# Kernel optimization log

Hardware: AMD Instinct MI355X
Metric: run time of the kernel (lower is better)

## Reference

```python
import jax, jax.numpy as jnp
import numpy as np

N = 65536
E = 1048576
NFEAT, NHID, NCLASS = 128, 64, 40


def setup_inputs() -> dict:
    key = jax.random.key(0)
    ks = jax.random.split(key, 20)
    inp = {
        "x": jax.random.normal(ks[0], (N, NFEAT), dtype=jnp.float32),
        "src": jax.random.randint(ks[1], (E,), 0, N, dtype=jnp.int32),
        "dst": jax.random.randint(ks[2], (E,), 0, N, dtype=jnp.int32),
        "edge_w": jax.random.uniform(ks[3], (E,), dtype=jnp.float32),
    }
    dims = [(NFEAT, NHID)] + [(NHID, NHID)] * 5 + [(NHID, NCLASS)]
    for i, (fi, fo) in enumerate(dims, start=1):
        scale = 1.0 / np.sqrt(fi)
        inp[f"W{i}"] = jax.random.uniform(ks[3 + i], (fi, fo), minval=-scale, maxval=scale, dtype=jnp.float32)
        inp[f"b{i}"] = jax.random.uniform(ks[10 + i], (fo,), minval=-scale, maxval=scale, dtype=jnp.float32)
    return inp


def _gc(h, W, b, src, dst, edge_w):
    # GraphConvolution: adj @ (h @ W) + b, with adj in COO form.
    support = h @ W                      # [N, fo] dense GEMM
    msgs = support[src] * edge_w[:, None]  # [E, fo] irregular gather
    agg = jax.ops.segment_sum(msgs, dst, num_segments=N)  # scatter-add
    return agg + b


def reference(x, src, dst, edge_w, W1, b1, W2, b2, W3, b3, W4, b4, W5, b5, W6, b6, W7, b7):
    # eval mode: dropout is identity
    h = jax.nn.relu(_gc(x, W1, b1, src, dst, edge_w))
    h = jax.nn.relu(_gc(h, W2, b2, src, dst, edge_w))
    h = jax.nn.relu(_gc(h, W3, b3, src, dst, edge_w)) + h
    h = jax.nn.relu(_gc(h, W4, b4, src, dst, edge_w)) + h
    h = jax.nn.relu(_gc(h, W5, b5, src, dst, edge_w)) + h
    h = jax.nn.relu(_gc(h, W6, b6, src, dst, edge_w))
    h = _gc(h, W7, b7, src, dst, edge_w)
    return jax.nn.log_softmax(h, axis=1)
```

## Files before the change

### kernel.cpp

```cpp
#include <hip/hip_runtime.h>
#include <math.h>


constexpr int NFEAT = 128, NHID = 64, NCLASS = 40;

typedef unsigned short ushort_t;
typedef int ivec4 __attribute__((ext_vector_type(4)));

__device__ inline float bf2f(ushort_t u) {
  union { unsigned int i; float f; } v; v.i = ((unsigned int)u) << 16; return v.f;
}
__device__ inline ushort_t f2bf(float f) {
  union { float f; unsigned int i; } v; v.f = f;
  unsigned int lsb = (v.i >> 16) & 1u;
  v.i += 0x7fffu + lsb;
  return (ushort_t)(v.i >> 16);
}

__global__ void rank_k(const int* __restrict__ dst, int* __restrict__ cnt4,
                       int* __restrict__ rank, int E, int N) {
  int i = blockIdx.x * blockDim.x + threadIdx.x;
  int base = i * 4;
  if (base >= E) return;
  int4 d4 = *(const int4*)(dst + base);
  int r0 = atomicAdd(&cnt4[0 * N + d4.x], 1);
  int r1 = atomicAdd(&cnt4[1 * N + d4.y], 1);
  int r2 = atomicAdd(&cnt4[2 * N + d4.z], 1);
  int r3 = atomicAdd(&cnt4[3 * N + d4.w], 1);
  ivec4 rr = { (r0 << 2) | 0, (r1 << 2) | 1, (r2 << 2) | 2, (r3 << 2) | 3 };
  __builtin_nontemporal_store(rr, (ivec4*)(rank + base));
}

__global__ void scan1_k(const int* __restrict__ cnt4, int* __restrict__ off,
                        int* __restrict__ bsum, int4* __restrict__ sb4, int n) {
  __shared__ int tmp[256];
  int tid = threadIdx.x;
  int i = blockIdx.x * 256 + tid;
  int c0 = 0, c1 = 0, c2 = 0, c3 = 0;
  if (i < n) {
    c0 = cnt4[i]; c1 = cnt4[n + i]; c2 = cnt4[2 * n + i]; c3 = cnt4[3 * n + i];
  }
  int v = c0 + c1 + c2 + c3;
  tmp[tid] = v;
  __syncthreads();
  for (int d = 1; d < 256; d <<= 1) {
    int t = (tid >= d) ? tmp[tid - d] : 0;
    __syncthreads();
    tmp[tid] += t;
    __syncthreads();
  }
  if (i < n) {
    off[i] = tmp[tid] - v;
    sb4[i] = make_int4(0, c0, c0 + c1, c0 + c1 + c2);
  }
  if (tid == 255) bsum[blockIdx.x] = tmp[255];
}

__global__ void scan2_k(int* __restrict__ bsum, int nb) {
  __shared__ int tmp[256];
  int tid = threadIdx.x;
  int v = (tid < nb) ? bsum[tid] : 0;
  tmp[tid] = v;
  __syncthreads();
  for (int d = 1; d < 256; d <<= 1) {
    int t = (tid >= d) ? tmp[tid - d] : 0;
    __syncthreads();
    tmp[tid] += t;
    __syncthreads();
  }
  if (tid < nb) bsum[tid] = tmp[tid] - v;
}

__global__ void scan3_k(int* __restrict__ off, const int* __restrict__ bsum, int n, int E) {
  int i = blockIdx.x * blockDim.x + threadIdx.x;
  if (i < n) off[i] += bsum[i >> 8];
  if (i == 0) off[n] = E;
}

__global__ void fill_k(const int* __restrict__ src, const int* __restrict__ dst,
                       const float* __restrict__ w, const int* __restrict__ off,
                       const int* __restrict__ rank, const int* __restrict__ sb4,
                       int2* __restrict__ edata, int E) {
  int i = blockIdx.x * blockDim.x + threadIdx.x;
  int base = i * 4;
  if (base >= E) return;
  int4 s4 = *(const int4*)(src + base);
  int4 d4 = *(const int4*)(dst + base);
  float4 w4 = *(const float4*)(w + base);
  int4 r4 = *(const int4*)(rank + base);
  int dd[4] = { d4.x, d4.y, d4.z, d4.w };
  int rr[4] = { r4.x, r4.y, r4.z, r4.w };
  int ss[4] = { s4.x, s4.y, s4.z, s4.w };
  float ww[4] = { w4.x, w4.y, w4.z, w4.w };
  int ob[4], sb[4];
#pragma unroll
  for (int k = 0; k < 4; ++k) ob[k] = off[dd[k]];
#pragma unroll
  for (int k = 0; k < 4; ++k) sb[k] = sb4[dd[k] * 4 + (rr[k] & 3)];
#pragma unroll
  for (int k = 0; k < 4; ++k) {
    int pos = ob[k] + sb[k] + (rr[k] >> 2);
    int2 v = make_int2(ss[k], __float_as_int(ww[k]));
    __builtin_nontemporal_store(*(const long long*)&v, (long long*)&edata[pos]);
  }
}

template<int FI, int FO>
__global__ __launch_bounds__(256) void gemm_k(const float* __restrict__ h,
                                              const float* __restrict__ W,
                                              ushort_t* __restrict__ out, int n) {
  constexpr int HS = 68;
  __shared__ float hl[64 * HS];
  __shared__ float wl[64 * 64];
  int tid = threadIdx.x;
  int row0 = blockIdx.x * 64;
  int tx = tid & 15, ty = tid >> 4;

  float acc[4][4] = {};

  for (int kc = 0; kc < FI; kc += 64) {
    {
      const float* hb = h + (size_t)row0 * FI + kc;
      for (int i = tid; i < 64 * 16; i += 256) {
        int r = i >> 4, kk = (i & 15) << 2;
        float4 v = *(const float4*)(hb + (size_t)r * FI + kk);
        *(float4*)&hl[r * HS + kk] = v;
      }
    }
    if (FO == 64) {
      const float4* Wb = (const float4*)(W + (size_t)kc * 64);
      for (int i = tid; i < 64 * 16; i += 256) ((float4*)wl)[i] = Wb[i];
    } else {
      for (int i = tid; i < 64 * 64; i += 256) wl[i] = 0.0f;
      __syncthreads();
      for (int i = tid; i < 64 * FO; i += 256)
        wl[(i / FO) * 64 + (i % FO)] = W[(size_t)(kc + i / FO) * FO + (i % FO)];
    }
    __syncthreads();

    for (int k4 = 0; k4 < 64; k4 += 4) {
      float4 a[4];
#pragma unroll
      for (int r = 0; r < 4; ++r)
        a[r] = *(const float4*)&hl[(ty * 4 + r) * HS + k4];
#pragma unroll
      for (int j = 0; j < 4; ++j) {
        float4 bv = *(const float4*)&wl[(k4 + j) * 64 + tx * 4];
        const float* bp = (const float*)&bv;
#pragma unroll
        for (int r = 0; r < 4; ++r) {
          const float* ap = (const float*)&a[r];
#pragma unroll
          for (int c = 0; c < 4; ++c) acc[r][c] += ap[j] * bp[c];
        }
      }
    }
    __syncthreads();
  }

  if (FO == 64) {
#pragma unroll
    for (int r = 0; r < 4; ++r) {
      ushort_t pk[4];
#pragma unroll
      for (int c = 0; c < 4; ++c) pk[c] = f2bf(acc[r][c]);
      *(ushort4*)&out[(size_t)(row0 + ty * 4 + r) * 64 + tx * 4] =
          make_ushort4(pk[0], pk[1], pk[2], pk[3]);
    }
  } else {
#pragma unroll
    for (int r = 0; r < 4; ++r)
#pragma unroll
      for (int c = 0; c < 4; ++c) {
        int col = tx * 4 + c;
        if (col < FO) out[(size_t)(row0 + ty * 4 + r) * FO + col] = f2bf(acc[r][c]);
      }
  }
}

__global__ __launch_bounds__(256, 4) void agg_k(
    const ushort_t* __restrict__ support,
    const int2* __restrict__ edata,
    const int* __restrict__ off,
    const float* __restrict__ bias,
    const float* __restrict__ resid,
    float* __restrict__ out,
    int n, int do_relu) {
  int tid = blockIdx.x * blockDim.x + threadIdx.x;
  int p = tid >> 6, lane = tid & 63;
  int nA = 2 * p, nB = 2 * p + 1;
  if (nA >= n) return;
  int half = lane >> 5;
  int hl   = lane & 31;
  int e0a = __builtin_amdgcn_readfirstlane(off[nA]);
  int e0b = __builtin_amdgcn_readfirstlane(off[nB]);
  int e1b = __builtin_amdgcn_readfirstlane(off[nB + 1]);
  int degA = e0b - e0a, degB = e1b - e0b;

  const ushort_t* sp = support + hl * 2;
  const int* epA = (const int*)(edata + e0a);
  const int* epB = (const int*)(edata + e0b);

  float axA[4] = {}, ayA[4] = {}, axB[4] = {}, ayB[4] = {};

  int sA[16], sB[16];
#pragma unroll
  for (int j = 0; j < 16; ++j) {
    int rel = 2 * j + half;
    sA[j] = epA[(rel < degA ? rel : 0) * 2];
  }
#pragma unroll
  for (int j = 0; j < 16; ++j) {
    int rel = 2 * j + half;
    sB[j] = epB[(rel < degB ? rel : 0) * 2];
  }
  unsigned int uA[16], uB[16];
#pragma unroll
  for (int j = 0; j < 16; ++j)
    uA[j] = *(const unsigned int*)(sp + ((size_t)sA[j] << 6));
#pragma unroll
  for (int j = 0; j < 16; ++j)
    uB[j] = *(const unsigned int*)(sp + ((size_t)sB[j] << 6));
#pragma unroll
  for (int j = 0; j < 16; ++j) {
    int rel = 2 * j + half;
    float w = (rel < degA) ? __int_as_float(epA[rel * 2 + 1]) : 0.0f;
    axA[j & 3] += w * __int_as_float(uA[j] << 16);
    ayA[j & 3] += w * __int_as_float(uA[j] & 0xffff0000u);
  }
#pragma unroll
  for (int j = 0; j < 16; ++j) {
    int rel = 2 * j + half;
    float w = (rel < degB) ? __int_as_float(epB[rel * 2 + 1]) : 0.0f;
    axB[j & 3] += w * __int_as_float(uB[j] << 16);
    ayB[j & 3] += w * __int_as_float(uB[j] & 0xffff0000u);
  }
  for (int it = 32; it < degA; it += 16) {
    int2 ed[8];
#pragma unroll
    for (int j = 0; j < 8; ++j) {
      int rel = it + 2 * j + half;
      ed[j] = *(const int2*)(epA + (rel < degA ? rel : 0) * 2);
    }
    unsigned int uu[8];
#pragma unroll
    for (int j = 0; j < 8; ++j)
      uu[j] = *(const unsigned int*)(sp + ((size_t)ed[j].x << 6));
#pragma unroll
    for (int j = 0; j < 8; ++j) {
      int rel = it + 2 * j + half;
      float w = (rel < degA) ? __int_as_float(ed[j].y) : 0.0f;
      axA[j & 3] += w * __int_as_float(uu[j] << 16);
      ayA[j & 3] += w * __int_as_float(uu[j] & 0xffff0000u);
    }
  }
  for (int it = 32; it < degB; it += 16) {
    int2 ed[8];
#pragma unroll
    for (int j = 0; j < 8; ++j) {
      int rel = it + 2 * j + half;
      ed[j] = *(const int2*)(epB + (rel < degB ? rel : 0) * 2);
    }
    unsigned int uu[8];
#pragma unroll
    for (int j = 0; j < 8; ++j)
      uu[j] = *(const unsigned int*)(sp + ((size_t)ed[j].x << 6));
#pragma unroll
    for (int j = 0; j < 8; ++j) {
      int rel = it + 2 * j + half;
      float w = (rel < degB) ? __int_as_float(ed[j].y) : 0.0f;
      axB[j & 3] += w * __int_as_float(uu[j] << 16);
      ayB[j & 3] += w * __int_as_float(uu[j] & 0xffff0000u);
    }
  }

  float sxA = ((axA[0] + axA[1]) + (axA[2] + axA[3]));
  float syA = ((ayA[0] + ayA[1]) + (ayA[2] + ayA[3]));
  float sxB = ((axB[0] + axB[1]) + (axB[2] + axB[3]));
  float syB = ((ayB[0] + ayB[1]) + (ayB[2] + ayB[3]));
  sxA += __shfl_xor(sxA, 32, 64);
  syA += __shfl_xor(syA, 32, 64);
  sxB += __shfl_xor(sxB, 32, 64);
  syB += __shfl_xor(syB, 32, 64);

  float2 bv = *(const float2*)&bias[hl * 2];
  if (half == 0) {
    float vx = sxA + bv.x, vy = syA + bv.y;
    if (do_relu) { vx = fmaxf(vx, 0.0f); vy = fmaxf(vy, 0.0f); }
    if (resid) {
      float2 r = *(const float2*)&resid[(size_t)nA * 64 + hl * 2];
      vx += r.x; vy += r.y;
    }
    *(float2*)&out[(size_t)nA * 64 + hl * 2] = make_float2(vx, vy);
  } else {
    float vx = sxB + bv.x, vy = syB + bv.y;
    if (do_relu) { vx = fmaxf(vx, 0.0f); vy = fmaxf(vy, 0.0f); }
    if (resid) {
      float2 r = *(const float2*)&resid[(size_t)nB * 64 + hl * 2];
      vx += r.x; vy += r.y;
    }
    *(float2*)&out[(size_t)nB * 64 + hl * 2] = make_float2(vx, vy);
  }
}

__global__ __launch_bounds__(256, 4) void agg_final_k(
    const ushort_t* __restrict__ support,
    const int2* __restrict__ edata,
    const int* __restrict__ off,
    const float* __restrict__ bias,
    float* __restrict__ out, int n) {
  int tid = blockIdx.x * blockDim.x + threadIdx.x;
  int p = tid >> 6, lane = tid & 63;
  int nA = 2 * p, nB = 2 * p + 1;
  if (nA >= n) return;
  int half = lane >> 5;
  int hl   = lane & 31;
  int col  = (hl < 20 ? hl : 0) * 2;
  int e0a = __builtin_amdgcn_readfirstlane(off[nA]);
  int e0b = __builtin_amdgcn_readfirstlane(off[nB]);
  int e1b = __builtin_amdgcn_readfirstlane(off[nB + 1]);
  int degA = e0b - e0a, degB = e1b - e0b;

  const ushort_t* sp = support + col;
  const int* epA = (const int*)(edata + e0a);
  const int* epB = (const int*)(edata + e0b);

  float axA[4] = {}, ayA[4] = {}, axB[4] = {}, ayB[4] = {};

  int sA[16], sB[16];
#pragma unroll
  for (int j = 0; j < 16; ++j) {
    int rel = 2 * j + half;
    sA[j] = epA[(rel < degA ? rel : 0) * 2];
  }
#pragma unroll
  for (int j = 0; j < 16; ++j) {
    int rel = 2 * j + half;
    sB[j] = epB[(rel < degB ? rel : 0) * 2];
  }
  unsigned int uA[16], uB[16];
#pragma unroll
  for (int j = 0; j < 16; ++j)
    uA[j] = *(const unsigned int*)(sp + (size_t)sA[j] * NCLASS);
#pragma unroll
  for (int j = 0; j < 16; ++j)
    uB[j] = *(const unsigned int*)(sp + (size_t)sB[j] * NCLASS);
#pragma unroll
  for (int j = 0; j < 16; ++j) {
    int rel = 2 * j + half;
    float w = (rel < degA) ? __int_as_float(epA[rel * 2 + 1]) : 0.0f;
    axA[j & 3] += w * __int_as_float(uA[j] << 16);
    ayA[j & 3] += w * __int_as_float(uA[j] & 0xffff0000u);
  }
#pragma unroll
  for (int j = 0; j < 16; ++j) {
    int rel = 2 * j + half;
    float w = (rel < degB) ? __int_as_float(epB[rel * 2 + 1]) : 0.0f;
    axB[j & 3] += w * __int_as_float(uB[j] << 16);
    ayB[j & 3] += w * __int_as_float(uB[j] & 0xffff0000u);
  }
  for (int it = 32; it < degA; it += 16) {
    int2 ed[8];
#pragma unroll
    for (int j = 0; j < 8; ++j) {
      int rel = it + 2 * j + half;
      ed[j] = *(const int2*)(epA + (rel < degA ? rel : 0) * 2);
    }
    unsigned int uu[8];
#pragma unroll
    for (int j = 0; j < 8; ++j)
      uu[j] = *(const unsigned int*)(sp + (size_t)ed[j].x * NCLASS);
#pragma unroll
    for (int j = 0; j < 8; ++j) {
      int rel = it + 2 * j + half;
      float w = (rel < degA) ? __int_as_float(ed[j].y) : 0.0f;
      axA[j & 3] += w * __int_as_float(uu[j] << 16);
      ayA[j & 3] += w * __int_as_float(uu[j] & 0xffff0000u);
    }
  }
  for (int it = 32; it < degB; it += 16) {
    int2 ed[8];
#pragma unroll
    for (int j = 0; j < 8; ++j) {
      int rel = it + 2 * j + half;
      ed[j] = *(const int2*)(epB + (rel < degB ? rel : 0) * 2);
    }
    unsigned int uu[8];
#pragma unroll
    for (int j = 0; j < 8; ++j)
      uu[j] = *(const unsigned int*)(sp + (size_t)ed[j].x * NCLASS);
#pragma unroll
    for (int j = 0; j < 8; ++j) {
      int rel = it + 2 * j + half;
      float w = (rel < degB) ? __int_as_float(ed[j].y) : 0.0f;
      axB[j & 3] += w * __int_as_float(uu[j] << 16);
      ayB[j & 3] += w * __int_as_float(uu[j] & 0xffff0000u);
    }
  }

  float sxA = ((axA[0] + axA[1]) + (axA[2] + axA[3]));
  float syA = ((ayA[0] + ayA[1]) + (ayA[2] + ayA[3]));
  float sxB = ((axB[0] + axB[1]) + (axB[2] + axB[3]));
  float syB = ((ayB[0] + ayB[1]) + (ayB[2] + ayB[3]));
  sxA += __shfl_xor(sxA, 32, 64);
  syA += __shfl_xor(syA, 32, 64);
  sxB += __shfl_xor(sxB, 32, 64);
  syB += __shfl_xor(syB, 32, 64);

  bool valid = (hl < 20);
  float2 bv = *(const float2*)&bias[col];
  float vxA = sxA + bv.x, vyA = syA + bv.y;
  float vxB = sxB + bv.x, vyB = syB + bv.y;

  float mA = valid ? fmaxf(vxA, vyA) : -INFINITY;
  float mB = valid ? fmaxf(vxB, vyB) : -INFINITY;
#pragma unroll
  for (int d = 32; d; d >>= 1) {
    mA = fmaxf(mA, __shfl_xor(mA, d, 64));
    mB = fmaxf(mB, __shfl_xor(mB, d, 64));
  }
  float exA = (valid && half == 0) ? (expf(vxA - mA) + expf(vyA - mA)) : 0.0f;
  float exB = (valid && half == 0) ? (expf(vxB - mB) + expf(vyB - mB)) : 0.0f;
  float sA2 = exA, sB2 = exB;
#pragma unroll
  for (int d = 32; d; d >>= 1) {
    sA2 += __shfl_xor(sA2, d, 64);
    sB2 += __shfl_xor(sB2, d, 64);
  }
  if (valid) {
    if (half == 0) {
      float ls = logf(sA2);
      *(float2*)&out[(size_t)nA * NCLASS + hl * 2] =
          make_float2(vxA - mA - ls, vyA - mA - ls);
    } else {
      float ls = logf(sB2);
      *(float2*)&out[(size_t)nB * NCLASS + hl * 2] =
          make_float2(vxB - mB - ls, vyB - mB - ls);
    }
  }
}

extern "C" void kernel_launch(void* const* d_in, const int* in_sizes, int n_in,
                              void* d_out, int out_size, void* d_ws, size_t ws_size,
                              hipStream_t stream) {
  const float* x   = (const float*)d_in[0];
  const int*   src = (const int*)d_in[1];
  const int*   dst = (const int*)d_in[2];
  const float* ew  = (const float*)d_in[3];
  const float* W[7]; const float* b[7];
  for (int i = 0; i < 7; ++i) {
    W[i] = (const float*)d_in[4 + 2 * i];
    b[i] = (const float*)d_in[5 + 2 * i];
  }
  int N = in_sizes[0] / NFEAT;
  int E = in_sizes[1];

  char* ws = (char*)d_ws;
  int*      off     = (int*)(ws + 0);
  int*      bsum    = (int*)(ws + (1ll << 20));
  int*      cnt4    = (int*)(ws + (2ll << 20));
  int4*     sb4     = (int4*)(ws + (3ll << 20));
  int2*     edata   = (int2*)(ws + (4ll << 20));
  int*      rank    = (int*)(ws + (12ll << 20));
  ushort_t* support = (ushort_t*)(ws + (16ll << 20));
  float*    hA      = (float*)(ws + (32ll << 20));
  float*    hB      = (float*)(ws + (48ll << 20));

  (void)hipMemsetAsync(cnt4, 0, (size_t)4 * N * sizeof(int), stream);
  rank_k<<<(E / 4 + 255) / 256, 256, 0, stream>>>(dst, cnt4, rank, E, N);
  int nb = (N + 255) / 256;
  scan1_k<<<nb, 256, 0, stream>>>(cnt4, off, bsum, sb4, N);
  scan2_k<<<1, 256, 0, stream>>>(bsum, nb);
  scan3_k<<<nb, 256, 0, stream>>>(off, bsum, N, E);
  fill_k<<<(E / 4 + 255) / 256, 256, 0, stream>>>(src, dst, ew, off, rank,
                                                  (const int*)sb4, edata, E);

  int gb_gemm = N / 64;
  int gb_agg  = N / 8;

  gemm_k<128, 64><<<gb_gemm, 256, 0, stream>>>(x, W[0], support, N);
  agg_k<<<gb_agg, 256, 0, stream>>>(support, edata, off, b[0], nullptr, hA, N, 1);
  gemm_k<64, 64><<<gb_gemm, 256, 0, stream>>>(hA, W[1], support, N);
  agg_k<<<gb_agg, 256, 0, stream>>>(support, edata, off, b[1], nullptr, hB, N, 1);
  gemm_k<64, 64><<<gb_gemm, 256, 0, stream>>>(hB, W[2], support, N);
  agg_k<<<gb_agg, 256, 0, stream>>>(support, edata, off, b[2], hB, hA, N, 1);
  gemm_k<64, 64><<<gb_gemm, 256, 0, stream>>>(hA, W[3], support, N);
  agg_k<<<gb_agg, 256, 0, stream>>>(support, edata, off, b[3], hA, hB, N, 1);
  gemm_k<64, 64><<<gb_gemm, 256, 0, stream>>>(hB, W[4], support, N);
  agg_k<<<gb_agg, 256, 0, stream>>>(support, edata, off, b[4], hB, hA, N, 1);
  gemm_k<64, 64><<<gb_gemm, 256, 0, stream>>>(hA, W[5], support, N);
  agg_k<<<gb_agg, 256, 0, stream>>>(support, edata, off, b[5], nullptr, hB, N, 1);
  gemm_k<64, 40><<<gb_gemm, 256, 0, stream>>>(hB, W[6], support, N);
  agg_final_k<<<gb_agg, 256, 0, stream>>>(support, edata, off, b[6], (float*)d_out, N);
}
```

Before: 403.4 us.

## Fuse next layer's dense GEMM into aggregation epilogue

Each aggregation kernel now loads the next layer's weight matrix into shared memory and, after computing a node's activated row, multiplies it by W to produce the next support row directly in bf16. This removes six standalone GEMM launches and the fp32 hidden-state round trip through global memory, writing h only when a later residual needs it. Support buffers ping-pong between two regions. The cost is extra per-wave FMA work and LDS use (16KB of weights per block), which may reduce occupancy in the latency-bound gather kernel.

```diff
diff --git a/kernel.cpp b/kernel.cpp
--- a/kernel.cpp
+++ b/kernel.cpp
@@ -127,14 +127,9 @@
         *(float4*)&hl[r * HS + kk] = v;
       }
     }
-    if (FO == 64) {
+    {
       const float4* Wb = (const float4*)(W + (size_t)kc * 64);
       for (int i = tid; i < 64 * 16; i += 256) ((float4*)wl)[i] = Wb[i];
-    } else {
-      for (int i = tid; i < 64 * 64; i += 256) wl[i] = 0.0f;
-      __syncthreads();
-      for (int i = tid; i < 64 * FO; i += 256)
-        wl[(i / FO) * 64 + (i % FO)] = W[(size_t)(kc + i / FO) * FO + (i % FO)];
     }
     __syncthreads();
 
@@ -158,38 +153,39 @@
     __syncthreads();
   }
 
-  if (FO == 64) {
-#pragma unroll
-    for (int r = 0; r < 4; ++r) {
-      ushort_t pk[4];
-#pragma unroll
-      for (int c = 0; c < 4; ++c) pk[c] = f2bf(acc[r][c]);
-      *(ushort4*)&out[(size_t)(row0 + ty * 4 + r) * 64 + tx * 4] =
-          make_ushort4(pk[0], pk[1], pk[2], pk[3]);
-    }
-  } else {
-#pragma unroll
-    for (int r = 0; r < 4; ++r)
-#pragma unroll
-      for (int c = 0; c < 4; ++c) {
-        int col = tx * 4 + c;
-        if (col < FO) out[(size_t)(row0 + ty * 4 + r) * FO + col] = f2bf(acc[r][c]);
-      }
-  }
-}
-
-__global__ __launch_bounds__(256, 4) void agg_k(
+#pragma unroll
+  for (int r = 0; r < 4; ++r) {
+    ushort_t pk[4];
+#pragma unroll
+    for (int c = 0; c < 4; ++c) pk[c] = f2bf(acc[r][c]);
+    *(ushort4*)&out[(size_t)(row0 + ty * 4 + r) * 64 + tx * 4] =
+        make_ushort4(pk[0], pk[1], pk[2], pk[3]);
+  }
+}
+
+template<int FO, bool WRITE_H>
+__global__ __launch_bounds__(256, 4) void aggemm_k(
     const ushort_t* __restrict__ support,
     const int2* __restrict__ edata,
     const int* __restrict__ off,
     const float* __restrict__ bias,
     const float* __restrict__ resid,
-    float* __restrict__ out,
-    int n, int do_relu) {
-  int tid = blockIdx.x * blockDim.x + threadIdx.x;
-  int p = tid >> 6, lane = tid & 63;
+    const float* __restrict__ Wn,
+    ushort_t* __restrict__ sout,
+    float* __restrict__ hout,
+    int n) {
+  __shared__ float Wl[64 * FO];
+  __shared__ float hls[4][2][64];
+  int tid = threadIdx.x;
+  for (int i = tid; i < (64 * FO) / 4; i += 256)
+    ((float4*)Wl)[i] = ((const float4*)Wn)[i];
+  __syncthreads();
+
+  int p = (blockIdx.x * blockDim.x + tid) >> 6, lane = tid & 63;
+  int wv = tid >> 6;
   int nA = 2 * p, nB = 2 * p + 1;
   if (nA >= n) return;
+  if (nB >= n) nB = n - 1;
   int half = lane >> 5;
   int hl   = lane & 31;
   int e0a = __builtin_amdgcn_readfirstlane(off[nA]);
@@ -283,24 +279,39 @@
   sxB += __shfl_xor(sxB, 32, 64);
   syB += __shfl_xor(syB, 32, 64);
 
+  int node = (half == 0) ? nA : nB;
   float2 bv = *(const float2*)&bias[hl * 2];
-  if (half == 0) {
-    float vx = sxA + bv.x, vy = syA + bv.y;
-    if (do_relu) { vx = fmaxf(vx, 0.0f); vy = fmaxf(vy, 0.0f); }
-    if (resid) {
-      float2 r = *(const float2*)&resid[(size_t)nA * 64 + hl * 2];
-      vx += r.x; vy += r.y;
-    }
-    *(float2*)&out[(size_t)nA * 64 + hl * 2] = make_float2(vx, vy);
-  } else {
-    float vx = sxB + bv.x, vy = syB + bv.y;
-    if (do_relu) { vx = fmaxf(vx, 0.0f); vy = fmaxf(vy, 0.0f); }
-    if (resid) {
-      float2 r = *(const float2*)&resid[(size_t)nB * 64 + hl * 2];
-      vx += r.x; vy += r.y;
-    }
-    *(float2*)&out[(size_t)nB * 64 + hl * 2] = make_float2(vx, vy);
-  }
+  float vx = ((half == 0) ? sxA : sxB) + bv.x;
+  float vy = ((half == 0) ? syA : syB) + bv.y;
+  vx = fmaxf(vx, 0.0f); vy = fmaxf(vy, 0.0f);
+  if (resid) {
+    float2 r = *(const float2*)&resid[(size_t)node * 64 + hl * 2];
+    vx += r.x; vy += r.y;
+  }
+  if (WRITE_H)
+    *(float2*)&hout[(size_t)node * 64 + hl * 2] = make_float2(vx, vy);
+  *(float2*)&hls[wv][half][hl * 2] = make_float2(vx, vy);
+  __threadfence_block();
+
+  int col2 = (2 * hl < FO) ? 2 * hl : 0;
+  const float* hb = hls[wv][half];
+  float ox0 = 0.f, ox1 = 0.f, oy0 = 0.f, oy1 = 0.f;
+#pragma unroll
+  for (int k = 0; k < 64; k += 4) {
+    float4 hv = *(const float4*)&hb[k];
+    float2 w0 = *(const float2*)&Wl[(k + 0) * FO + col2];
+    float2 w1 = *(const float2*)&Wl[(k + 1) * FO + col2];
+    float2 w2 = *(const float2*)&Wl[(k + 2) * FO + col2];
+    float2 w3 = *(const float2*)&Wl[(k + 3) * FO + col2];
+    ox0 += hv.x * w0.x; oy0 += hv.x * w0.y;
+    ox1 += hv.y * w1.x; oy1 += hv.y * w1.y;
+    ox0 += hv.z * w2.x; oy0 += hv.z * w2.y;
+    ox1 += hv.w * w3.x; oy1 += hv.w * w3.y;
+  }
+  float ox = ox0 + ox1, oy = oy0 + oy1;
+  unsigned int pk = (unsigned int)f2bf(ox) | ((unsigned int)f2bf(oy) << 16);
+  if (2 * hl < FO)
+    *(unsigned int*)&sout[(size_t)node * FO + 2 * hl] = pk;
 }
 
 __global__ __launch_bounds__(256, 4) void agg_final_k(
@@ -313,6 +324,7 @@
   int p = tid >> 6, lane = tid & 63;
   int nA = 2 * p, nB = 2 * p + 1;
   if (nA >= n) return;
+  if (nB >= n) nB = n - 1;
   int half = lane >> 5;
   int hl   = lane & 31;
   int col  = (hl < 20 ? hl : 0) * 2;
@@ -462,7 +474,8 @@
   int4*     sb4     = (int4*)(ws + (3ll << 20));
   int2*     edata   = (int2*)(ws + (4ll << 20));
   int*      rank    = (int*)(ws + (12ll << 20));
-  ushort_t* support = (ushort_t*)(ws + (16ll << 20));
+  ushort_t* SA      = (ushort_t*)(ws + (16ll << 20));
+  ushort_t* SB      = (ushort_t*)(ws + (24ll << 20));
   float*    hA      = (float*)(ws + (32ll << 20));
   float*    hB      = (float*)(ws + (48ll << 20));
 
@@ -478,18 +491,18 @@
   int gb_gemm = N / 64;
   int gb_agg  = N / 8;
 
-  gemm_k<128, 64><<<gb_gemm, 256, 0, stream>>>(x, W[0], support, N);
-  agg_k<<<gb_agg, 256, 0, stream>>>(support, edata, off, b[0], nullptr, hA, N, 1);
-  gemm_k<64, 64><<<gb_gemm, 256, 0, stream>>>(hA, W[1], support, N);
-  agg_k<<<gb_agg, 256, 0, stream>>>(support, edata, off, b[1], nullptr, hB, N, 1);
-  gemm_k<64, 64><<<gb_gemm, 256, 0, stream>>>(hB, W[2], support, N);
-  agg_k<<<gb_agg, 256, 0, stream>>>(support, edata, off, b[2], hB, hA, N, 1);
-  gemm_k<64, 64><<<gb_gemm, 256, 0, stream>>>(hA, W[3], support, N);
-  agg_k<<<gb_agg, 256, 0, stream>>>(support, edata, off, b[3], hA, hB, N, 1);
-  gemm_k<64, 64><<<gb_gemm, 256, 0, stream>>>(hB, W[4], support, N);
-  agg_k<<<gb_agg, 256, 0, stream>>>(support, edata, off, b[4], hB, hA, N, 1);
-  gemm_k<64, 64><<<gb_gemm, 256, 0, stream>>>(hA, W[5], support, N);
-  agg_k<<<gb_agg, 256, 0, stream>>>(support, edata, off, b[5], nullptr, hB, N, 1);
-  gemm_k<64, 40><<<gb_gemm, 256, 0, stream>>>(hB, W[6], support, N);
-  agg_final_k<<<gb_agg, 256, 0, stream>>>(support, edata, off, b[6], (float*)d_out, N);
-}
+  gemm_k<128, 64><<<gb_gemm, 256, 0, stream>>>(x, W[0], SA, N);
+  aggemm_k<64, false><<<gb_agg, 256, 0, stream>>>(SA, edata, off, b[0], nullptr,
+                                                  W[1], SB, nullptr, N);
+  aggemm_k<64, true><<<gb_agg, 256, 0, stream>>>(SB, edata, off, b[1], nullptr,
+                                                 W[2], SA, hA, N);
+  aggemm_k<64, true><<<gb_agg, 256, 0, stream>>>(SA, edata, off, b[2], hA,
+                                                 W[3], SB, hB, N);
+  aggemm_k<64, true><<<gb_agg, 256, 0, stream>>>(SB, edata, off, b[3], hB,
+                                                 W[4], SA, hA, N);
+  aggemm_k<64, false><<<gb_agg, 256, 0, stream>>>(SA, edata, off, b[4], hA,
+                                                  W[5], SB, nullptr, N);
+  aggemm_k<40, false><<<gb_agg, 256, 0, stream>>>(SB, edata, off, b[5], nullptr,
+                                                  W[6], SA, nullptr, N);
+  agg_final_k<<<gb_agg, 256, 0, stream>>>(SA, edata, off, b[6], (float*)d_out, N);
+}
```

Result: faster. 386.8 us (-4.1%).
